# Kernel tuning notes

Measured on AMD Instinct MI355X. Metric: run time of the kernel, lower is better.

The kernel has to match this reference:

```python
import math
import jax, jax.numpy as jnp
import numpy as np

B, D_MODEL, SEQ_LEN = 8, 1024, 4096
EMB_DIM, ORDER = 3, 64
TARGET, FAST_PCT, SLOW_PCT = 0.01, 0.3, 1.5  # ExponentialModulation defaults


def _pos_emb(L):
    # PositionalEmbedding buffers built for SEQ_LEN, sliced to L
    bands = (EMB_DIM - 1) // 2
    t = jnp.linspace(0.0, 1.0, SEQ_LEN)[None, :, None]                 # [1,S,1]
    t_r = jnp.linspace(0.0, SEQ_LEN - 1.0, SEQ_LEN)[None, :, None]
    w_ang = 2.0 * math.pi * t_r / SEQ_LEN                              # [1,S,1]
    f = jnp.linspace(1e-4, float(bands - 1), bands)[None, None, :]     # [1,1,bands]
    ph = f * w_ang                                                      # [1,S,bands]
    # z = exp(-1j*f*w): real = cos(ph), imag = -sin(ph)
    z = jnp.concatenate([t, jnp.cos(ph), -jnp.sin(ph)], axis=-1)        # [1,S,EMB_DIM]
    return z[:, :L], t[:, :L]


def setup_inputs() -> dict:
    key = jax.random.key(0)
    ks = jax.random.split(key, 9)
    s = 0.2  # small init scale for MLP weights
    return {
        "x": jax.random.normal(ks[0], (B, D_MODEL, SEQ_LEN), jnp.float32),
        "bias_param": jax.random.normal(ks[1], (D_MODEL,), jnp.float32),
        "W1": jax.random.normal(ks[2], (EMB_DIM, ORDER), jnp.float32) * s,
        "b1": jax.random.normal(ks[3], (ORDER,), jnp.float32) * s,
        "W2": jax.random.normal(ks[4], (ORDER, ORDER), jnp.float32) * s,
        "b2": jax.random.normal(ks[5], (ORDER,), jnp.float32) * s,
        "W3": jax.random.normal(ks[6], (ORDER, ORDER), jnp.float32) * s,
        "b3": jax.random.normal(ks[7], (ORDER,), jnp.float32) * s,
        "Wout": jax.random.normal(ks[8], (ORDER, D_MODEL), jnp.float32) * s,
        "freq": jnp.ones((ORDER,), jnp.float32),  # Sin freq, w=1 (shared across all Sin acts)
        "L": SEQ_LEN,
    }


def reference(x, bias_param, W1, b1, W2, b2, W3, b3, Wout, freq, L):
    # ---- implicit filter: k = MLP(pos_emb) * exp_modulation ----
    z, t = _pos_emb(L)                       # [1,L,EMB_DIM], [1,L,1]
    h = jnp.sin(freq * (z @ W1 + b1))        # shared Sin activation
    h = jnp.sin(freq * (h @ W2 + b2))
    h = jnp.sin(freq * (h @ W3 + b3))
    h = h @ Wout                             # [1,L,D]
    max_d = math.log(TARGET) / FAST_PCT
    min_d = math.log(TARGET) / SLOW_PCT
    deltas = jnp.abs(jnp.linspace(min_d, max_d, D_MODEL))[None, None, :]
    k = (h * jnp.exp(-t * deltas))[0].T      # [D,L] per-channel filters
    # ---- FFT long convolution with residual bias path (gelu=False) ----
    N = 2 * L
    u_f = jnp.fft.rfft(x, n=N)               # [B,D,N/2+1]
    k_f = jnp.fft.rfft(k, n=N)               # [D,N/2+1]
    y = jnp.fft.irfft(u_f * k_f, n=N)[..., :L]
    out = y + x * bias_param[:, None]
    return out.astype(x.dtype)
```

## Files before the change

### kernel.cpp

```cpp
#include <hip/hip_runtime.h>
#include <math.h>

#define SEQ    4096
#define NFFT   8192
#define DMODEL 1024
#define ORDER  64
#define CT     512
#define MLPT   256

typedef float2 cf;

#define ZI(c) ((c) ^ ((((c) >> 4) & 7) << 1))

__device__ __forceinline__ cf cadd(cf a, cf b) { return make_float2(a.x + b.x, a.y + b.y); }
__device__ __forceinline__ cf csub(cf a, cf b) { return make_float2(a.x - b.x, a.y - b.y); }
__device__ __forceinline__ cf cmul(cf a, cf b) { return make_float2(a.x * b.x - a.y * b.y, a.x * b.y + a.y * b.x); }
__device__ __forceinline__ cf cmulj(cf a, cf b) { return make_float2(a.x * b.x + a.y * b.y, a.y * b.x - a.x * b.y); }

#define RT2 0.70710678118654752f

template<bool INV> __device__ __forceinline__ cf tw8_1(cf d) {
    if (!INV) return make_float2(RT2 * (d.x + d.y), RT2 * (d.y - d.x));
    else      return make_float2(RT2 * (d.x - d.y), RT2 * (d.y + d.x));
}
template<bool INV> __device__ __forceinline__ cf tw8_2(cf d) {
    if (!INV) return make_float2(d.y, -d.x);
    else      return make_float2(-d.y, d.x);
}
template<bool INV> __device__ __forceinline__ cf tw8_3(cf d) {
    if (!INV) return make_float2(RT2 * (d.y - d.x), -RT2 * (d.x + d.y));
    else      return make_float2(-RT2 * (d.x + d.y), RT2 * (d.x - d.y));
}

template<bool INV>
__device__ __forceinline__ void dft4(cf& x0, cf& x1, cf& x2, cf& x3) {
    cf A = cadd(x0, x2), B = csub(x0, x2);
    cf C = cadd(x1, x3), D = csub(x1, x3);
    x0 = cadd(A, C); x2 = csub(A, C);
    if (!INV) { x1 = make_float2(B.x + D.y, B.y - D.x); x3 = make_float2(B.x - D.y, B.y + D.x); }
    else      { x1 = make_float2(B.x - D.y, B.y + D.x); x3 = make_float2(B.x + D.y, B.y - D.x); }
}

template<bool INV>
__device__ __forceinline__ void dft8(cf v[8]) {
    cf s0 = cadd(v[0], v[4]), s1 = cadd(v[1], v[5]), s2 = cadd(v[2], v[6]), s3 = cadd(v[3], v[7]);
    cf d0 = csub(v[0], v[4]), d1 = csub(v[1], v[5]), d2 = csub(v[2], v[6]), d3 = csub(v[3], v[7]);
    cf t1 = tw8_1<INV>(d1), t2 = tw8_2<INV>(d2), t3 = tw8_3<INV>(d3);
    dft4<INV>(s0, s1, s2, s3);
    dft4<INV>(d0, t1, t2, t3);
    v[0] = s0; v[2] = s1; v[4] = s2; v[6] = s3;
    v[1] = d0; v[3] = t1; v[5] = t2; v[7] = t3;
}

#define TW_CHAIN(w1, w2, w3, w4, w5, w6, w7) \
    cf w2 = cmul(w1, w1); cf w3 = cmul(w2, w1); cf w4 = cmul(w2, w2); \
    cf w5 = cmul(w3, w2); cf w6 = cmul(w3, w3); cf w7 = cmul(w4, w3);

template<int L, int S>
__device__ __forceinline__ void stage_fwd(float2* z, const cf* __restrict__ tw) {
    int t = threadIdx.x;
    int j0 = 2 * (t & (L / 2 - 1));
    int base = (t / (L / 2)) * (8 * L);
    int c0 = base + j0;
    cf a[8], b[8];
    #pragma unroll
    for (int k = 0; k < 8; k++) {
        float4 p = *(const float4*)&z[ZI(c0 + k * L)];
        a[k] = make_float2(p.x, p.y); b[k] = make_float2(p.z, p.w);
    }
    dft8<false>(a); dft8<false>(b);
    cf wA1 = tw[S * j0], wB1 = tw[S * j0 + S];
    TW_CHAIN(wA1, wA2, wA3, wA4, wA5, wA6, wA7)
    TW_CHAIN(wB1, wB2, wB3, wB4, wB5, wB6, wB7)
    a[1] = cmul(a[1], wA1); b[1] = cmul(b[1], wB1);
    a[2] = cmul(a[2], wA2); b[2] = cmul(b[2], wB2);
    a[3] = cmul(a[3], wA3); b[3] = cmul(b[3], wB3);
    a[4] = cmul(a[4], wA4); b[4] = cmul(b[4], wB4);
    a[5] = cmul(a[5], wA5); b[5] = cmul(b[5], wB5);
    a[6] = cmul(a[6], wA6); b[6] = cmul(b[6], wB6);
    a[7] = cmul(a[7], wA7); b[7] = cmul(b[7], wB7);
    #pragma unroll
    for (int k = 0; k < 8; k++)
        *(float4*)&z[ZI(c0 + k * L)] = make_float4(a[k].x, a[k].y, b[k].x, b[k].y);
    __syncthreads();
}

template<int L, int S4>
__device__ __forceinline__ void c4_fwd(float2* z, const cf* __restrict__ tw) {
    int t = threadIdx.x;
    int j = t & (L - 1);
    int c0 = (t / L) * (8 * L) + j;
    cf a[8];
    #pragma unroll
    for (int k = 0; k < 8; k++) a[k] = z[ZI(c0 + k * L)];
    dft8<false>(a);
    cf w1 = tw[S4 * j], w = w1;
    a[1] = cmul(a[1], w);
    #pragma unroll
    for (int k = 2; k < 8; k++) { w = cmul(w, w1); a[k] = cmul(a[k], w); }
    #pragma unroll
    for (int k = 0; k < 8; k++) z[ZI(c0 + k * L)] = a[k];
    __syncthreads();
}

template<int L, int S4>
__device__ __forceinline__ void c4_inv(float2* z, const cf* __restrict__ tw) {
    int t = threadIdx.x;
    int j = t & (L - 1);
    int c0 = (t / L) * (8 * L) + j;
    cf a[8];
    #pragma unroll
    for (int k = 0; k < 8; k++) a[k] = z[ZI(c0 + k * L)];
    cf w1 = tw[S4 * j], w = w1;
    a[1] = cmulj(a[1], w);
    #pragma unroll
    for (int k = 2; k < 8; k++) { w = cmul(w, w1); a[k] = cmulj(a[k], w); }
    dft8<true>(a);
    #pragma unroll
    for (int k = 0; k < 8; k++) z[ZI(c0 + k * L)] = a[k];
    __syncthreads();
}

__global__ void mlp_kernel(const float* __restrict__ W1, const float* __restrict__ b1,
                           const float* __restrict__ W2, const float* __restrict__ b2,
                           const float* __restrict__ W3, const float* __restrict__ b3,
                           const float* __restrict__ freq, float* __restrict__ Ht,
                           cf* __restrict__ tw) {
    if (blockIdx.x < NFFT / MLPT) {
        int j = blockIdx.x * MLPT + threadIdx.x;
        double ang = (2.0 * M_PI / (double)NFFT) * (double)j;
        tw[j] = make_float2((float)cos(ang), (float)(-sin(ang)));
    }

    int o = threadIdx.x & 63;
    int p = threadIdx.x >> 6;
    int l = blockIdx.x * 4 + p;
    __shared__ float hs[4][ORDER];

    float t   = (float)l / 4095.0f;
    float ang = 1e-4f * (float)(2.0 * M_PI) * (float)l / 4096.0f;
    float z0 = t, z1 = cosf(ang), z2 = -sinf(ang);
    float fo = freq[o];

    float a = z0 * W1[o] + z1 * W1[ORDER + o] + z2 * W1[2 * ORDER + o] + b1[o];
    hs[p][o] = sinf(fo * a);
    __syncthreads();

    a = b2[o];
    #pragma unroll
    for (int i = 0; i < ORDER; i++) a += hs[p][i] * W2[i * ORDER + o];
    float h2 = sinf(fo * a);
    __syncthreads();
    hs[p][o] = h2;
    __syncthreads();

    a = b3[o];
    #pragma unroll
    for (int i = 0; i < ORDER; i++) a += hs[p][i] * W3[i * ORDER + o];
    Ht[o * SEQ + l] = sinf(fo * a);
}

__global__ __launch_bounds__(MLPT) void kgen2_kernel(const float* __restrict__ Wout,
                                                     const float* __restrict__ Ht,
                                                     float* __restrict__ kfil) {
    __shared__ float Hs[ORDER][68];
    __shared__ float Ws[ORDER][68];
    int t  = threadIdx.x;
    int dt = blockIdx.x & 15, lt = blockIdx.x >> 4;

    #pragma unroll
    for (int r = 0; r < 4; r++) {
        int idx = t + 256 * r;
        int o = idx >> 4, c4 = (idx & 15) * 4;
        *(float4*)&Hs[o][c4] = *(const float4*)&Ht[o * SEQ + lt * 64 + c4];
        *(float4*)&Ws[o][c4] = *(const float4*)&Wout[o * DMODEL + dt * 64 + c4];
    }
    __syncthreads();

    int lq = (t & 15) * 4;
    int dq = (t >> 4) * 4;
    float acc[4][4] = {{0.f}};
    #pragma unroll 8
    for (int o = 0; o < ORDER; o++) {
        float4 h = *(float4*)&Hs[o][lq];
        float4 w = *(float4*)&Ws[o][dq];
        acc[0][0] += w.x * h.x; acc[0][1] += w.x * h.y; acc[0][2] += w.x * h.z; acc[0][3] += w.x * h.w;
        acc[1][0] += w.y * h.x; acc[1][1] += w.y * h.y; acc[1][2] += w.y * h.z; acc[1][3] += w.y * h.w;
        acc[2][0] += w.z * h.x; acc[2][1] += w.z * h.y; acc[2][2] += w.z * h.z; acc[2][3] += w.z * h.w;
        acc[3][0] += w.w * h.x; acc[3][1] += w.w * h.y; acc[3][2] += w.w * h.z; acc[3][3] += w.w * h.w;
    }

    const float MIN_D = -3.0701134573253944f;
    const float MAX_D = -15.350567286626971f;
    int l0 = lt * 64 + lq;
    #pragma unroll
    for (int di = 0; di < 4; di++) {
        int d = dt * 64 + dq + di;
        float delta = fabsf(MIN_D + (MAX_D - MIN_D) * (float)d / 1023.0f);
        float4 o4;
        o4.x = acc[di][0] * expf(-((float)(l0 + 0) / 4095.0f) * delta);
        o4.y = acc[di][1] * expf(-((float)(l0 + 1) / 4095.0f) * delta);
        o4.z = acc[di][2] * expf(-((float)(l0 + 2) / 4095.0f) * delta);
        o4.w = acc[di][3] * expf(-((float)(l0 + 3) / 4095.0f) * delta);
        *(float4*)&kfil[(size_t)d * SEQ + l0] = o4;
    }
}

__global__ __launch_bounds__(MLPT) void kfft2_kernel(const float* __restrict__ kfil,
                                                     const cf* __restrict__ tw,
                                                     cf* __restrict__ Ke,
                                                     cf* __restrict__ Ko) {
    int d = blockIdx.x, t = threadIdx.x;
    __shared__ __align__(16) float2 z2[SEQ];

    const float2* kf2 = (const float2*)(kfil + (size_t)d * SEQ);
    for (int rep = 0; rep < 2; rep++) {
        if (rep) __syncthreads();
        #pragma unroll
        for (int m = 0; m < 8; m++) {
            int s = t + 256 * m;
            float2 kk = kf2[s];
            if (rep == 0) {
                *(float4*)&z2[ZI(2 * s)] = make_float4(kk.x, 0.f, kk.y, 0.f);
            } else {
                cf w0 = tw[2 * s], w1 = tw[2 * s + 1];
                *(float4*)&z2[ZI(2 * s)] = make_float4(kk.x * w0.x, kk.x * w0.y,
                                                       kk.y * w1.x, kk.y * w1.y);
            }
        }
        __syncthreads();

        stage_fwd<512, 2>(z2, tw);
        stage_fwd<64, 16>(z2, tw);
        stage_fwd<8, 128>(z2, tw);

        {
            int c0 = 16 * t;
            cf v[16];
            #pragma unroll
            for (int i = 0; i < 8; i++) {
                float4 p = *(const float4*)&z2[ZI(c0 + 2 * i)];
                v[2 * i] = make_float2(p.x, p.y); v[2 * i + 1] = make_float2(p.z, p.w);
            }
            dft8<false>(v); dft8<false>(v + 8);
            const float sc = 1.0f / (float)NFFT;
            float4* K4 = (float4*)((rep ? Ko : Ke) + (size_t)d * SEQ + c0);
            #pragma unroll
            for (int i = 0; i < 8; i++)
                K4[i] = make_float4(v[2 * i].x * sc, v[2 * i].y * sc,
                                    v[2 * i + 1].x * sc, v[2 * i + 1].y * sc);
        }
    }
}

__global__ __launch_bounds__(CT, 4) void conv_kernel(const float* __restrict__ x,
                                                     const float* __restrict__ bias,
                                                     const cf* __restrict__ Ke,
                                                     const cf* __restrict__ Ko,
                                                     const cf* __restrict__ tw,
                                                     float* __restrict__ out) {
    int wg = blockIdx.x;
    int d = wg & (DMODEL - 1);
    int pair = wg >> 10;
    int t = threadIdx.x;

    const float* xa = x + ((size_t)(2 * pair) * DMODEL + d) * SEQ;
    const float* xb = x + ((size_t)(2 * pair + 1) * DMODEL + d) * SEQ;

    __shared__ __align__(16) float2 z[SEQ];

    cf zr[8], u[8];
    #pragma unroll
    for (int k = 0; k < 8; k++) {
        int n = t + 512 * k;
        zr[k] = make_float2(xa[n], xb[n]);
    }

    for (int sel = 0; sel < 2; sel++) {
        {
            cf a[8];
            if (sel == 0) {
                #pragma unroll
                for (int k = 0; k < 8; k++) a[k] = zr[k];
            } else {
                #pragma unroll
                for (int k = 0; k < 8; k++) a[k] = cmul(zr[k], tw[t + 512 * k]);
            }
            dft8<false>(a);
            cf w1 = tw[2 * t], w = w1;
            a[1] = cmul(a[1], w);
            #pragma unroll
            for (int k = 2; k < 8; k++) { w = cmul(w, w1); a[k] = cmul(a[k], w); }
            #pragma unroll
            for (int k = 0; k < 8; k++) z[ZI(t + 512 * k)] = a[k];
        }
        __syncthreads();

        c4_fwd<64, 16>(z, tw);
        c4_fwd<8, 128>(z, tw);

        {
            int c0 = 8 * t;
            cf v[8];
            #pragma unroll
            for (int i = 0; i < 4; i++) {
                float4 p = *(const float4*)&z[ZI(c0 + 2 * i)];
                v[2 * i] = make_float2(p.x, p.y); v[2 * i + 1] = make_float2(p.z, p.w);
            }
            dft8<false>(v);
            const float4* K4 = (const float4*)((sel ? Ko : Ke) + (size_t)d * SEQ + c0);
            #pragma unroll
            for (int i = 0; i < 4; i++) {
                float4 kk = K4[i];
                v[2 * i]     = cmul(v[2 * i],     make_float2(kk.x, kk.y));
                v[2 * i + 1] = cmul(v[2 * i + 1], make_float2(kk.z, kk.w));
            }
            dft8<true>(v);
            #pragma unroll
            for (int i = 0; i < 4; i++)
                *(float4*)&z[ZI(c0 + 2 * i)] = make_float4(v[2 * i].x, v[2 * i].y,
                                                           v[2 * i + 1].x, v[2 * i + 1].y);
        }
        __syncthreads();

        c4_inv<8, 128>(z, tw);
        c4_inv<64, 16>(z, tw);

        {
            cf a[8];
            #pragma unroll
            for (int k = 0; k < 8; k++) a[k] = z[ZI(t + 512 * k)];
            cf w1 = tw[2 * t], w = w1;
            a[1] = cmulj(a[1], w);
            #pragma unroll
            for (int k = 2; k < 8; k++) { w = cmul(w, w1); a[k] = cmulj(a[k], w); }
            dft8<true>(a);

            if (sel == 0) {
                #pragma unroll
                for (int k = 0; k < 8; k++) u[k] = a[k];
            } else {
                float bd = bias[d];
                float* oa = out + ((size_t)(2 * pair) * DMODEL + d) * SEQ;
                float* ob = out + ((size_t)(2 * pair + 1) * DMODEL + d) * SEQ;
                #pragma unroll
                for (int k = 0; k < 8; k++) {
                    int n = t + 512 * k;
                    cf q = cmulj(a[k], tw[n]);
                    float yx = u[k].x + q.x;
                    float yy = u[k].y + q.y;
                    oa[n] = yx + bd * zr[k].x;
                    ob[n] = yy + bd * zr[k].y;
                }
            }
        }
        __syncthreads();
    }
}

extern "C" void kernel_launch(void* const* d_in, const int* in_sizes, int n_in,
                              void* d_out, int out_size, void* d_ws, size_t ws_size,
                              hipStream_t stream) {
    (void)in_sizes; (void)n_in; (void)out_size; (void)ws_size;
    const float* x    = (const float*)d_in[0];
    const float* bias = (const float*)d_in[1];
    const float* W1   = (const float*)d_in[2];
    const float* b1   = (const float*)d_in[3];
    const float* W2   = (const float*)d_in[4];
    const float* b2   = (const float*)d_in[5];
    const float* W3   = (const float*)d_in[6];
    const float* b3   = (const float*)d_in[7];
    const float* Wout = (const float*)d_in[8];
    const float* freq = (const float*)d_in[9];
    float* out = (float*)d_out;

    float* wsf  = (float*)d_ws;
    float* Ht   = wsf;
    cf*    tw   = (cf*)(wsf + 262144);
    float* kfil = wsf + 262144 + 16384;
    cf*    Ke   = (cf*)(wsf + 262144 + 16384 + 4194304);
    cf*    Ko   = (cf*)(wsf + 262144 + 16384 + 4194304 + 8388608);

    hipLaunchKernelGGL(mlp_kernel, dim3(SEQ / 4), dim3(MLPT), 0, stream,
                       W1, b1, W2, b2, W3, b3, freq, Ht, tw);
    hipLaunchKernelGGL(kgen2_kernel, dim3(1024), dim3(MLPT), 0, stream, Wout, Ht, kfil);
    hipLaunchKernelGGL(kfft2_kernel, dim3(DMODEL), dim3(MLPT), 0, stream, kfil, tw, Ke, Ko);
    hipLaunchKernelGGL(conv_kernel, dim3(DMODEL * 4), dim3(CT), 0, stream,
                       x, bias, Ke, Ko, tw, out);
}
```

Measured before the change: 197.3 us.

## Process even and odd FFT halves together in interleaved shared buffer

Replaces the two sequential passes (even/odd halves of the 8192-point transform) with a single pass that carries both halves per thread, storing them interleaved as float4 in a doubled shared-memory buffer. This halves the number of barriers and passes, and turns shared-memory accesses into wider float4 operations. In exchange it doubles the LDS footprint to 64KB per block and raises register pressure, which may reduce occupancy under the existing launch bounds.

```diff
diff --git a/kernel.cpp b/kernel.cpp
--- a/kernel.cpp
+++ b/kernel.cpp
@@ -86,38 +86,52 @@
 }
 
 template<int L, int S4>
-__device__ __forceinline__ void c4_fwd(float2* z, const cf* __restrict__ tw) {
+__device__ __forceinline__ void p_fwd(float2* zz, const cf* __restrict__ tw) {
     int t = threadIdx.x;
     int j = t & (L - 1);
-    int c0 = (t / L) * (8 * L) + j;
-    cf a[8];
-    #pragma unroll
-    for (int k = 0; k < 8; k++) a[k] = z[ZI(c0 + k * L)];
-    dft8<false>(a);
+    int m0 = (t / L) * (8 * L) + j;
+    cf aA[8], aB[8];
+    #pragma unroll
+    for (int k = 0; k < 8; k++) {
+        float4 p = *(const float4*)&zz[ZI(2 * (m0 + k * L))];
+        aA[k] = make_float2(p.x, p.y); aB[k] = make_float2(p.z, p.w);
+    }
+    dft8<false>(aA); dft8<false>(aB);
     cf w1 = tw[S4 * j], w = w1;
-    a[1] = cmul(a[1], w);
-    #pragma unroll
-    for (int k = 2; k < 8; k++) { w = cmul(w, w1); a[k] = cmul(a[k], w); }
-    #pragma unroll
-    for (int k = 0; k < 8; k++) z[ZI(c0 + k * L)] = a[k];
+    aA[1] = cmul(aA[1], w); aB[1] = cmul(aB[1], w);
+    #pragma unroll
+    for (int k = 2; k < 8; k++) {
+        w = cmul(w, w1);
+        aA[k] = cmul(aA[k], w); aB[k] = cmul(aB[k], w);
+    }
+    #pragma unroll
+    for (int k = 0; k < 8; k++)
+        *(float4*)&zz[ZI(2 * (m0 + k * L))] = make_float4(aA[k].x, aA[k].y, aB[k].x, aB[k].y);
     __syncthreads();
 }
 
 template<int L, int S4>
-__device__ __forceinline__ void c4_inv(float2* z, const cf* __restrict__ tw) {
+__device__ __forceinline__ void p_inv(float2* zz, const cf* __restrict__ tw) {
     int t = threadIdx.x;
     int j = t & (L - 1);
-    int c0 = (t / L) * (8 * L) + j;
-    cf a[8];
-    #pragma unroll
-    for (int k = 0; k < 8; k++) a[k] = z[ZI(c0 + k * L)];
+    int m0 = (t / L) * (8 * L) + j;
+    cf aA[8], aB[8];
+    #pragma unroll
+    for (int k = 0; k < 8; k++) {
+        float4 p = *(const float4*)&zz[ZI(2 * (m0 + k * L))];
+        aA[k] = make_float2(p.x, p.y); aB[k] = make_float2(p.z, p.w);
+    }
     cf w1 = tw[S4 * j], w = w1;
-    a[1] = cmulj(a[1], w);
-    #pragma unroll
-    for (int k = 2; k < 8; k++) { w = cmul(w, w1); a[k] = cmulj(a[k], w); }
-    dft8<true>(a);
-    #pragma unroll
-    for (int k = 0; k < 8; k++) z[ZI(c0 + k * L)] = a[k];
+    aA[1] = cmulj(aA[1], w); aB[1] = cmulj(aB[1], w);
+    #pragma unroll
+    for (int k = 2; k < 8; k++) {
+        w = cmul(w, w1);
+        aA[k] = cmulj(aA[k], w); aB[k] = cmulj(aB[k], w);
+    }
+    dft8<true>(aA); dft8<true>(aB);
+    #pragma unroll
+    for (int k = 0; k < 8; k++)
+        *(float4*)&zz[ZI(2 * (m0 + k * L))] = make_float4(aA[k].x, aA[k].y, aB[k].x, aB[k].y);
     __syncthreads();
 }
 
@@ -267,94 +281,97 @@
     const float* xa = x + ((size_t)(2 * pair) * DMODEL + d) * SEQ;
     const float* xb = x + ((size_t)(2 * pair + 1) * DMODEL + d) * SEQ;
 
-    __shared__ __align__(16) float2 z[SEQ];
-
-    cf zr[8], u[8];
+    __shared__ __align__(16) float2 zz[2 * SEQ];
+
+    cf zr[8];
     #pragma unroll
     for (int k = 0; k < 8; k++) {
         int n = t + 512 * k;
         zr[k] = make_float2(xa[n], xb[n]);
     }
 
-    for (int sel = 0; sel < 2; sel++) {
-        {
-            cf a[8];
-            if (sel == 0) {
-                #pragma unroll
-                for (int k = 0; k < 8; k++) a[k] = zr[k];
-            } else {
-                #pragma unroll
-                for (int k = 0; k < 8; k++) a[k] = cmul(zr[k], tw[t + 512 * k]);
-            }
-            dft8<false>(a);
-            cf w1 = tw[2 * t], w = w1;
-            a[1] = cmul(a[1], w);
-            #pragma unroll
-            for (int k = 2; k < 8; k++) { w = cmul(w, w1); a[k] = cmul(a[k], w); }
-            #pragma unroll
-            for (int k = 0; k < 8; k++) z[ZI(t + 512 * k)] = a[k];
-        }
-        __syncthreads();
-
-        c4_fwd<64, 16>(z, tw);
-        c4_fwd<8, 128>(z, tw);
-
-        {
-            int c0 = 8 * t;
-            cf v[8];
-            #pragma unroll
-            for (int i = 0; i < 4; i++) {
-                float4 p = *(const float4*)&z[ZI(c0 + 2 * i)];
-                v[2 * i] = make_float2(p.x, p.y); v[2 * i + 1] = make_float2(p.z, p.w);
-            }
-            dft8<false>(v);
-            const float4* K4 = (const float4*)((sel ? Ko : Ke) + (size_t)d * SEQ + c0);
-            #pragma unroll
-            for (int i = 0; i < 4; i++) {
-                float4 kk = K4[i];
-                v[2 * i]     = cmul(v[2 * i],     make_float2(kk.x, kk.y));
-                v[2 * i + 1] = cmul(v[2 * i + 1], make_float2(kk.z, kk.w));
-            }
-            dft8<true>(v);
-            #pragma unroll
-            for (int i = 0; i < 4; i++)
-                *(float4*)&z[ZI(c0 + 2 * i)] = make_float4(v[2 * i].x, v[2 * i].y,
-                                                           v[2 * i + 1].x, v[2 * i + 1].y);
-        }
-        __syncthreads();
-
-        c4_inv<8, 128>(z, tw);
-        c4_inv<64, 16>(z, tw);
-
-        {
-            cf a[8];
-            #pragma unroll
-            for (int k = 0; k < 8; k++) a[k] = z[ZI(t + 512 * k)];
-            cf w1 = tw[2 * t], w = w1;
-            a[1] = cmulj(a[1], w);
-            #pragma unroll
-            for (int k = 2; k < 8; k++) { w = cmul(w, w1); a[k] = cmulj(a[k], w); }
-            dft8<true>(a);
-
-            if (sel == 0) {
-                #pragma unroll
-                for (int k = 0; k < 8; k++) u[k] = a[k];
-            } else {
-                float bd = bias[d];
-                float* oa = out + ((size_t)(2 * pair) * DMODEL + d) * SEQ;
-                float* ob = out + ((size_t)(2 * pair + 1) * DMODEL + d) * SEQ;
-                #pragma unroll
-                for (int k = 0; k < 8; k++) {
-                    int n = t + 512 * k;
-                    cf q = cmulj(a[k], tw[n]);
-                    float yx = u[k].x + q.x;
-                    float yy = u[k].y + q.y;
-                    oa[n] = yx + bd * zr[k].x;
-                    ob[n] = yy + bd * zr[k].y;
-                }
-            }
-        }
-        __syncthreads();
+    {
+        cf aA[8], aB[8];
+        #pragma unroll
+        for (int k = 0; k < 8; k++) {
+            aA[k] = zr[k];
+            aB[k] = cmul(zr[k], tw[t + 512 * k]);
+        }
+        dft8<false>(aA); dft8<false>(aB);
+        cf w1 = tw[2 * t], w = w1;
+        aA[1] = cmul(aA[1], w); aB[1] = cmul(aB[1], w);
+        #pragma unroll
+        for (int k = 2; k < 8; k++) {
+            w = cmul(w, w1);
+            aA[k] = cmul(aA[k], w); aB[k] = cmul(aB[k], w);
+        }
+        #pragma unroll
+        for (int k = 0; k < 8; k++) {
+            int m = t + 512 * k;
+            *(float4*)&zz[ZI(2 * m)] = make_float4(aA[k].x, aA[k].y, aB[k].x, aB[k].y);
+        }
+    }
+    __syncthreads();
+
+    p_fwd<64, 16>(zz, tw);
+    p_fwd<8, 128>(zz, tw);
+
+    {
+        int m0 = 8 * t;
+        cf vA[8], vB[8];
+        #pragma unroll
+        for (int i = 0; i < 8; i++) {
+            float4 p = *(const float4*)&zz[ZI(2 * (m0 + i))];
+            vA[i] = make_float2(p.x, p.y); vB[i] = make_float2(p.z, p.w);
+        }
+        dft8<false>(vA); dft8<false>(vB);
+        const float4* KE4 = (const float4*)(Ke + (size_t)d * SEQ + m0);
+        const float4* KO4 = (const float4*)(Ko + (size_t)d * SEQ + m0);
+        #pragma unroll
+        for (int i = 0; i < 4; i++) {
+            float4 ke = KE4[i];
+            vA[2 * i]     = cmul(vA[2 * i],     make_float2(ke.x, ke.y));
+            vA[2 * i + 1] = cmul(vA[2 * i + 1], make_float2(ke.z, ke.w));
+            float4 ko = KO4[i];
+            vB[2 * i]     = cmul(vB[2 * i],     make_float2(ko.x, ko.y));
+            vB[2 * i + 1] = cmul(vB[2 * i + 1], make_float2(ko.z, ko.w));
+        }
+        dft8<true>(vA); dft8<true>(vB);
+        #pragma unroll
+        for (int i = 0; i < 8; i++)
+            *(float4*)&zz[ZI(2 * (m0 + i))] = make_float4(vA[i].x, vA[i].y, vB[i].x, vB[i].y);
+    }
+    __syncthreads();
+
+    p_inv<8, 128>(zz, tw);
+    p_inv<64, 16>(zz, tw);
+
+    {
+        cf aA[8], aB[8];
+        #pragma unroll
+        for (int k = 0; k < 8; k++) {
+            float4 p = *(const float4*)&zz[ZI(2 * (t + 512 * k))];
+            aA[k] = make_float2(p.x, p.y); aB[k] = make_float2(p.z, p.w);
+        }
+        cf w1 = tw[2 * t], w = w1;
+        aA[1] = cmulj(aA[1], w); aB[1] = cmulj(aB[1], w);
+        #pragma unroll
+        for (int k = 2; k < 8; k++) {
+            w = cmul(w, w1);
+            aA[k] = cmulj(aA[k], w); aB[k] = cmulj(aB[k], w);
+        }
+        dft8<true>(aA); dft8<true>(aB);
+
+        float bd = bias[d];
+        float* oa = out + ((size_t)(2 * pair) * DMODEL + d) * SEQ;
+        float* ob = out + ((size_t)(2 * pair + 1) * DMODEL + d) * SEQ;
+        #pragma unroll
+        for (int k = 0; k < 8; k++) {
+            int n = t + 512 * k;
+            cf q = cmulj(aB[k], tw[n]);
+            oa[n] = aA[k].x + q.x + bd * zr[k].x;
+            ob[n] = aA[k].y + q.y + bd * zr[k].y;
+        }
     }
 }
 
```

New measurement: 222.5 us. 12.8% more time.
